# Optimization experiments

Measured on AMD Instinct MI355X. Metric: run time of the kernel, lower is better.

## Reference

```python
import jax, jax.numpy as jnp
import numpy as np

B, NA, NB = 2, 2048, 2048
DIM_A, DIM_B = 256, 256
HEADS, DH_A, DH_B = 8, 64, 64
INNER_A, INNER_B = DH_A * HEADS, DH_B * HEADS
EPS = 1e-5


def layer_norm(x, w, b):
    m = jnp.mean(x, axis=-1, keepdims=True)
    v = jnp.mean(jnp.square(x - m), axis=-1, keepdims=True)
    return (x - m) * jax.lax.rsqrt(v + EPS) * w + b


def setup_inputs() -> dict:
    key = jax.random.key(0)
    ks = jax.random.split(key, 16)
    s = 0.02
    return {
        "feat_a": jax.random.normal(ks[0], (B, NA, DIM_A), jnp.float32),
        "feat_b": jax.random.normal(ks[1], (B, NB, DIM_B), jnp.float32),
        "mask_a_b": jax.random.bernoulli(ks[2], 0.5, (B, NA, NB)),
        # linear weights stored (in, out)
        "Wq": jax.random.normal(ks[3], (DIM_A, INNER_B), jnp.float32) * s,
        "bq": jnp.zeros((INNER_B,), jnp.float32),
        "Wk": jax.random.normal(ks[4], (DIM_B, INNER_B), jnp.float32) * s,
        "bk": jnp.zeros((INNER_B,), jnp.float32),
        "Wv": jax.random.normal(ks[5], (DIM_B, INNER_A), jnp.float32) * s,
        "bv": jnp.zeros((INNER_A,), jnp.float32),
        "Wg": jax.random.normal(ks[6], (DIM_A, INNER_A), jnp.float32) * s,
        "bg": jnp.zeros((INNER_A,), jnp.float32),
        "Wo": jax.random.normal(ks[7], (INNER_A, DIM_A), jnp.float32) * s,
        "bo": jnp.zeros((DIM_A,), jnp.float32),
        "ln_a_w": jnp.ones((DIM_A,), jnp.float32),
        "ln_a_b": jnp.zeros((DIM_A,), jnp.float32),
        "ln_b_w": jnp.ones((DIM_B,), jnp.float32),
        "ln_b_b": jnp.zeros((DIM_B,), jnp.float32),
        "qln_w": jnp.ones((INNER_B,), jnp.float32),
        "qln_b": jnp.zeros((INNER_B,), jnp.float32),
        "kln_w": jnp.ones((INNER_B,), jnp.float32),
        "kln_b": jnp.zeros((INNER_B,), jnp.float32),
    }


def reference(feat_a, feat_b, mask_a_b, Wq, bq, Wk, bk, Wv, bv, Wg, bg, Wo, bo,
              ln_a_w, ln_a_b, ln_b_w, ln_b_b, qln_w, qln_b, kln_w, kln_b):
    scale = DH_B ** -0.5
    fa = layer_norm(feat_a, ln_a_w, ln_a_b)            # (b, na, dim_a)
    fb = layer_norm(feat_b, ln_b_w, ln_b_b)            # (b, nb, dim_b)
    q = layer_norm(fa @ Wq + bq, qln_w, qln_b)         # (b, na, inner_b)
    k = layer_norm(fb @ Wk + bk, kln_w, kln_b)         # (b, nb, inner_b)
    v = fb @ Wv + bv                                   # (b, nb, inner_a)
    g = fa @ Wg + bg                                   # (b, na, inner_a)
    q = q.reshape(B, NA, HEADS, DH_B)
    k = k.reshape(B, NB, HEADS, DH_B)
    v = v.reshape(B, NB, HEADS, DH_A)
    g = g.reshape(B, NA, HEADS, DH_A)
    sim = jnp.einsum('bihd,bjhd->bhij', q, k) * scale  # (b, h, na, nb)
    neg = jnp.finfo(sim.dtype).min
    sim = jnp.where(mask_a_b[:, None, :, :], sim, neg)
    attn = jax.nn.softmax(sim, axis=-1)
    out = jnp.einsum('bhij,bjhd->bihd', attn, v)       # (b, na, h, dh_a)
    out = jax.nn.sigmoid(g) * out
    out = out.reshape(B, NA, INNER_A)
    return out @ Wo + bo                               # (b, na, dim_a)
```

## Files before the change

### kernel.cpp

```cpp
#include <hip/hip_runtime.h>
#include <hip/hip_bf16.h>

using bf16 = __hip_bfloat16;
typedef short bf16x8 __attribute__((ext_vector_type(8)));
typedef float f32x4 __attribute__((ext_vector_type(4)));
typedef unsigned short ushort8_t __attribute__((ext_vector_type(8)));
typedef unsigned long long u64;

static constexpr int NA_ = 2048, NB_ = 2048;
static constexpr int H_ = 8, DH_ = 64, INNER_ = 512;
static constexpr int MROWS = 2 * NA_;

#define MFMA32(a, b, c) __builtin_amdgcn_mfma_f32_16x16x32_bf16(a, b, c, 0, 0, 0)

__device__ __forceinline__ unsigned short bfbits(float x) {
  bf16 h = __float2bfloat16(x);
  return __builtin_bit_cast(unsigned short, h);
}
__device__ __forceinline__ float b2f(unsigned short u) {
  unsigned v = ((unsigned)u) << 16;
  return __builtin_bit_cast(float, v);
}

__global__ __launch_bounds__(256) void prep_kernel(
    const float* __restrict__ fa_in, const float* __restrict__ fb_in,
    const float* __restrict__ law, const float* __restrict__ lab,
    const float* __restrict__ lbw, const float* __restrict__ lbb,
    bf16* __restrict__ fa, bf16* __restrict__ fb,
    const float* __restrict__ Wq, const float* __restrict__ Wk,
    const float* __restrict__ Wv, const float* __restrict__ Wg,
    const float* __restrict__ Wo,
    bf16* __restrict__ Wqt, bf16* __restrict__ Wkt,
    bf16* __restrict__ Wvt, bf16* __restrict__ Wgt,
    bf16* __restrict__ Woth, bf16* __restrict__ Wotl,
    const void* __restrict__ maskp, u64* __restrict__ mbits) {
  int blk = blockIdx.x;
  int t = threadIdx.x;
  if (blk < 2048) {
    int row = blk * 4 + (t >> 6);
    int lane = t & 63;
    const float *src, *w, *bb;
    bf16* dst;
    int r;
    if (row < MROWS) { src = fa_in; w = law; bb = lab; dst = fa; r = row; }
    else             { src = fb_in; w = lbw; bb = lbb; dst = fb; r = row - MROWS; }
    float4 x = *(const float4*)(src + (size_t)r * 256 + lane * 4);
    float s  = (x.x + x.y) + (x.z + x.w);
    float s2 = (x.x * x.x + x.y * x.y) + (x.z * x.z + x.w * x.w);
#pragma unroll
    for (int m = 32; m >= 1; m >>= 1) { s += __shfl_xor(s, m); s2 += __shfl_xor(s2, m); }
    float mean = s * (1.0f / 256.0f);
    float var  = s2 * (1.0f / 256.0f) - mean * mean;
    float rstd = rsqrtf(var + 1e-5f);
    float4 wv = *(const float4*)(w + lane * 4);
    float4 bv = *(const float4*)(bb + lane * 4);
    ushort4 o;
    o.x = bfbits((x.x - mean) * rstd * wv.x + bv.x);
    o.y = bfbits((x.y - mean) * rstd * wv.y + bv.y);
    o.z = bfbits((x.z - mean) * rstd * wv.z + bv.z);
    o.w = bfbits((x.w - mean) * rstd * wv.w + bv.w);
    *(ushort4*)(dst + (size_t)r * 256 + lane * 4) = o;
  } else if (blk < 4608) {
    int z = (blk - 2048) >> 9;
    int idx = ((blk - 2048) & 511) * 256 + t;
    if (z < 4) {
      const float* W = (z == 0) ? Wq : (z == 1) ? Wk : (z == 2) ? Wv : Wg;
      bf16* Wt = (z == 0) ? Wqt : (z == 1) ? Wkt : (z == 2) ? Wvt : Wgt;
      int kk = idx >> 9, n = idx & 511;
      Wt[n * 256 + kk] = __float2bfloat16(W[idx]);
    } else {
      int kk = idx >> 8, n = idx & 255;
      float w = Wo[idx];
      bf16 hi = __float2bfloat16(w);
      Woth[n * 512 + kk] = hi;
      Wotl[n * 512 + kk] = __float2bfloat16(w - __bfloat162float(hi));
    }
  } else {
    __shared__ unsigned shf[4];
    const unsigned char* mu = (const unsigned char*)maskp;
    bool nz = ((t & 3) != 0) && (mu[t] != 0);
    u64 bal = __ballot(nz);
    if ((t & 63) == 0) shf[t >> 6] = (bal != 0ull) ? 1u : 0u;
    __syncthreads();
    bool m8 = (shf[0] | shf[1] | shf[2] | shf[3]) != 0;
    int lane = t & 63, wid = t >> 6;
    int lb = blk - 4608;
    for (size_t word = (size_t)lb * 4 + wid; word < 131072; word += 8192) {
      size_t e = word * 64 + lane;
      int v = m8 ? (int)mu[e] : ((const int*)maskp)[e];
      u64 b2 = __ballot(v != 0);
      if (lane == 0) mbits[word] = b2;
    }
  }
}

__global__ __launch_bounds__(256) void gemm4_kernel(
    const bf16* __restrict__ fa, const bf16* __restrict__ fb,
    const bf16* __restrict__ Wqt, const bf16* __restrict__ Wkt,
    const bf16* __restrict__ Wgt, const bf16* __restrict__ Wvt,
    const float* __restrict__ bq, const float* __restrict__ bk,
    const float* __restrict__ bg, const float* __restrict__ bv,
    const float* __restrict__ qlw, const float* __restrict__ qlb,
    const float* __restrict__ klw, const float* __restrict__ klb,
    bf16* __restrict__ qo, bf16* __restrict__ ko,
    bf16* __restrict__ gout, bf16* __restrict__ vout) {
  __shared__ __align__(16) char sm[27648];
  int z = blockIdx.z;
  int t = threadIdx.x, wave = t >> 6, lane = t & 63;
  int lm = lane & 15, quad = lane >> 4, q8 = quad * 8;

  if (z < 2) {
    bf16* As = (bf16*)sm;
    float* Pred = (float*)(sm + 16896);
    float* MV   = (float*)(sm + 17408);
    const bf16* A    = z ? fb : fa;
    const bf16* Wt   = z ? Wkt : Wqt;
    const float* bias = z ? bk : bq;
    const float* lw  = z ? klw : qlw;
    const float* lb  = z ? klb : qlb;
    bf16* out        = z ? ko : qo;
    int m0 = blockIdx.x * 16;
#pragma unroll
    for (int i = 0; i < 2; i++) {
      int id = t + 256 * i, r = id >> 5, cg = id & 31;
      *(ushort8_t*)(&As[r * 264 + cg * 8]) =
          *(const ushort8_t*)(A + (size_t)(m0 + r) * 256 + cg * 8);
    }
    __syncthreads();
    int n0w = wave * 128;
    f32x4 acc[8] = {};
    const bf16* wrow[8];
#pragma unroll
    for (int ni = 0; ni < 8; ni++) wrow[ni] = Wt + (size_t)(n0w + ni * 16 + lm) * 256;
#pragma unroll
    for (int ks = 0; ks < 8; ks++) {
      int k0 = ks * 32;
      bf16x8 af = *(const bf16x8*)(&As[lm * 264 + k0 + q8]);
#pragma unroll
      for (int ni = 0; ni < 8; ni++) {
        bf16x8 bf_ = *(const bf16x8*)(wrow[ni] + k0 + q8);
        acc[ni] = MFMA32(af, bf_, acc[ni]);
      }
    }
    float bvv[8];
#pragma unroll
    for (int ni = 0; ni < 8; ni++) bvv[ni] = bias[n0w + ni * 16 + lm];
#pragma unroll
    for (int ni = 0; ni < 8; ni++)
#pragma unroll
      for (int r = 0; r < 4; r++) acc[ni][r] += bvv[ni];
#pragma unroll
    for (int r = 0; r < 4; r++) {
      float s = 0.f, s2 = 0.f;
#pragma unroll
      for (int ni = 0; ni < 8; ni++) { s += acc[ni][r]; s2 += acc[ni][r] * acc[ni][r]; }
#pragma unroll
      for (int m = 1; m <= 8; m <<= 1) { s += __shfl_xor(s, m); s2 += __shfl_xor(s2, m); }
      if (lm == 0) {
        int row = quad * 4 + r;
        Pred[row * 8 + wave * 2]     = s;
        Pred[row * 8 + wave * 2 + 1] = s2;
      }
    }
    __syncthreads();
    if (t < 16) {
      float s = 0.f, s2 = 0.f;
#pragma unroll
      for (int w = 0; w < 4; w++) { s += Pred[t * 8 + w * 2]; s2 += Pred[t * 8 + w * 2 + 1]; }
      float mean = s * (1.0f / 512.0f);
      float var  = s2 * (1.0f / 512.0f) - mean * mean;
      MV[t * 2]     = mean;
      MV[t * 2 + 1] = rsqrtf(var + 1e-5f);
    }
    __syncthreads();
    float lww[8], lbb_[8];
#pragma unroll
    for (int ni = 0; ni < 8; ni++) {
      lww[ni]  = lw[n0w + ni * 16 + lm];
      lbb_[ni] = lb[n0w + ni * 16 + lm];
    }
#pragma unroll
    for (int r = 0; r < 4; r++) {
      int row = quad * 4 + r;
      float mean = MV[row * 2], rstd = MV[row * 2 + 1];
      size_t obase = (size_t)(m0 + row) * 512 + n0w;
#pragma unroll
      for (int ni = 0; ni < 8; ni++)
        out[obase + ni * 16 + lm] =
            __float2bfloat16((acc[ni][r] - mean) * rstd * lww[ni] + lbb_[ni]);
    }
  } else {
    bf16* As = (bf16*)sm;
    bf16* Bs = (bf16*)(sm + 18432);
    const bf16* A    = (z == 3) ? fb : fa;
    const bf16* Wt   = (z == 3) ? Wvt : Wgt;
    const float* bias = (z == 3) ? bv : bg;
    int x = blockIdx.x;
    int m0 = (x >> 3) * 128, n0 = (x & 7) * 64;
    int wm = wave * 32;
    f32x4 acc[2][4] = {};
    for (int k0 = 0; k0 < 256; k0 += 64) {
      __syncthreads();
#pragma unroll
      for (int i = 0; i < 4; i++) {
        int id = t + 256 * i, r = id >> 3, cg = id & 7;
        *(ushort8_t*)(&As[r * 72 + cg * 8]) =
            *(const ushort8_t*)(A + (size_t)(m0 + r) * 256 + k0 + cg * 8);
      }
#pragma unroll
      for (int i = 0; i < 2; i++) {
        int id = t + 256 * i, r = id >> 3, cg = id & 7;
        *(ushort8_t*)(&Bs[r * 72 + cg * 8]) =
            *(const ushort8_t*)(Wt + (size_t)(n0 + r) * 256 + k0 + cg * 8);
      }
      __syncthreads();
#pragma unroll
      for (int kk = 0; kk < 64; kk += 32) {
        bf16x8 af[2], bf_[4];
#pragma unroll
        for (int mi = 0; mi < 2; mi++)
          af[mi] = *(const bf16x8*)(&As[(wm + mi * 16 + lm) * 72 + kk + q8]);
#pragma unroll
        for (int ni = 0; ni < 4; ni++)
          bf_[ni] = *(const bf16x8*)(&Bs[(ni * 16 + lm) * 72 + kk + q8]);
#pragma unroll
        for (int mi = 0; mi < 2; mi++)
#pragma unroll
          for (int ni = 0; ni < 4; ni++)
            acc[mi][ni] = MFMA32(af[mi], bf_[ni], acc[mi][ni]);
      }
    }
    if (z == 2) {
#pragma unroll
      for (int mi = 0; mi < 2; mi++)
#pragma unroll
        for (int ni = 0; ni < 4; ni++) {
          int nn = n0 + ni * 16 + lm;
          float bvv = bias[nn];
          int mb = m0 + wm + mi * 16 + quad * 4;
#pragma unroll
          for (int r = 0; r < 4; r++)
            gout[(size_t)(mb + r) * 512 + nn] = __float2bfloat16(acc[mi][ni][r] + bvv);
        }
    } else {
      __syncthreads();
      bf16* buf = (bf16*)sm;
#pragma unroll
      for (int mi = 0; mi < 2; mi++)
#pragma unroll
        for (int ni = 0; ni < 4; ni++) {
          int d_local = ni * 16 + lm;
          float bvv = bias[n0 + d_local];
          int j_local = wm + mi * 16 + quad * 4;
#pragma unroll
          for (int r = 0; r < 4; r++)
            buf[d_local * 136 + j_local + r] = __float2bfloat16(acc[mi][ni][r] + bvv);
        }
      __syncthreads();
      int bidx2 = m0 >> 11, j0g = m0 & 2047, hh = n0 >> 6;
      int dl = t >> 2, jseg = (t & 3) * 32;
      bf16* dstrow = vout + (size_t)((bidx2 * 8 + hh) * 64 + dl) * 2048 + j0g + jseg;
#pragma unroll
      for (int c = 0; c < 4; c++)
        *(ushort8_t*)(dstrow + c * 8) = *(const ushort8_t*)(&buf[dl * 136 + jseg + c * 8]);
    }
  }
}

__global__ __launch_bounds__(512) void attn_kernel(
    const bf16* __restrict__ q, const bf16* __restrict__ k,
    const bf16* __restrict__ vt, const bf16* __restrict__ g,
    const u64* __restrict__ mbits,
    bf16* __restrict__ gh, bf16* __restrict__ gl) {
  __shared__ __align__(16) char smem[65024];
  bf16* Qs = (bf16*)smem;
  bf16* KsB = (bf16*)(smem + 9216);
  bf16* VsB = (bf16*)(smem + 27648);
  bf16* PsB = (bf16*)(smem + 46080);
  float* Om = (float*)(smem + 9216);
  float* Lbuf = (float*)(smem + 64512);

  int qt = blockIdx.x, bh = blockIdx.y;
  int bidx = bh >> 3, h = bh & 7;
  int i0 = qt * 64;
  int t = threadIdx.x, wave = t >> 6, lane = t & 63;
  int jhalf = wave >> 2, w4 = wave & 3;
  int lm = lane & 15, quad = lane >> 4, q8 = quad * 8;
  int lt = t & 255;

  {
    int r = t >> 3, cg = t & 7;
    *(ushort8_t*)(&Qs[r * 72 + cg * 8]) =
        *(const ushort8_t*)(q + (size_t)(bidx * NA_ + i0 + r) * INNER_ + h * DH_ + cg * 8);
  }
  __syncthreads();
  bf16x8 bq0 = *(const bf16x8*)(&Qs[(w4 * 16 + lm) * 72 + q8]);
  bf16x8 bq1 = *(const bf16x8*)(&Qs[(w4 * 16 + lm) * 72 + 32 + q8]);

  f32x4 oacc[4] = {};
  float psum = 0.f;
  const float scale2 = 0.125f * 1.44269504088896f;

  const bf16* kb = k + (size_t)(bidx * NB_) * INNER_ + h * DH_;
  const bf16* vb = vt + (size_t)(bh * DH_) * NB_;
  bf16* Pw = PsB + wave * (16 * 72);
  bf16* Ks = KsB + jhalf * (64 * 72);
  bf16* Vs = VsB + jhalf * (64 * 72);
  const u64* mrp = mbits + ((size_t)(bidx * NA_ + i0 + w4 * 16 + lm)) * (NB_ / 64) + jhalf * 16;

  for (int it = 0; it < 16; it++) {
    int j0 = jhalf * 1024 + it * 64;
    __syncthreads();
#pragma unroll
    for (int i = 0; i < 2; i++) {
      int id = lt + 256 * i, r = id >> 3, cg = id & 7;
      *(ushort8_t*)(&Ks[r * 72 + cg * 8]) =
          *(const ushort8_t*)(kb + (size_t)(j0 + r) * INNER_ + cg * 8);
      *(ushort8_t*)(&Vs[r * 72 + cg * 8]) =
          *(const ushort8_t*)(vb + (size_t)r * NB_ + j0 + cg * 8);
    }
    u64 sm = mrp[it] >> (quad * 4);
    __syncthreads();

    f32x4 st[4];
#pragma unroll
    for (int nt = 0; nt < 4; nt++) {
      bf16x8 a0 = *(const bf16x8*)(&Ks[(nt * 16 + lm) * 72 + q8]);
      bf16x8 a1 = *(const bf16x8*)(&Ks[(nt * 16 + lm) * 72 + 32 + q8]);
      f32x4 a = {0.f, 0.f, 0.f, 0.f};
      a = MFMA32(a0, bq0, a);
      a = MFMA32(a1, bq1, a);
      st[nt] = a;
    }

    float pr[4][4];
#pragma unroll
    for (int nt = 0; nt < 4; nt++)
#pragma unroll
      for (int r = 0; r < 4; r++) {
        float p = exp2f(st[nt][r] * scale2 - 16.0f);
        unsigned live = (unsigned)(sm >> (nt * 16 + r)) & 1u;
        pr[nt][r] = live ? p : 0.0f;
      }

    float s0 = (pr[0][0] + pr[0][1]) + (pr[0][2] + pr[0][3]);
    float s1 = (pr[1][0] + pr[1][1]) + (pr[1][2] + pr[1][3]);
    float s2 = (pr[2][0] + pr[2][1]) + (pr[2][2] + pr[2][3]);
    float s3 = (pr[3][0] + pr[3][1]) + (pr[3][2] + pr[3][3]);
    psum += (s0 + s1) + (s2 + s3);

#pragma unroll
    for (int nt = 0; nt < 4; nt++) {
      ushort4 pk;
      pk.x = bfbits(pr[nt][0]);
      pk.y = bfbits(pr[nt][1]);
      pk.z = bfbits(pr[nt][2]);
      pk.w = bfbits(pr[nt][3]);
      *(ushort4*)(Pw + lm * 72 + nt * 16 + quad * 4) = pk;
    }

    bf16x8 ap0 = *(const bf16x8*)(&Pw[lm * 72 + q8]);
    bf16x8 ap1 = *(const bf16x8*)(&Pw[lm * 72 + 32 + q8]);
#pragma unroll
    for (int c = 0; c < 4; c++) {
      bf16x8 v0 = *(const bf16x8*)(&Vs[(c * 16 + lm) * 72 + q8]);
      bf16x8 v1 = *(const bf16x8*)(&Vs[(c * 16 + lm) * 72 + 32 + q8]);
      oacc[c] = MFMA32(ap0, v0, oacc[c]);
      oacc[c] = MFMA32(ap1, v1, oacc[c]);
    }
  }

  psum += __shfl_xor(psum, 16);
  psum += __shfl_xor(psum, 32);

  __syncthreads();
  if (quad == 0) Lbuf[jhalf * 64 + w4 * 16 + lm] = psum;
  if (jhalf == 1) {
#pragma unroll
    for (int c = 0; c < 4; c++)
#pragma unroll
      for (int r = 0; r < 4; r++)
        Om[w4 * (16 * 66) + (quad * 4 + r) * 66 + c * 16 + lm] = oacc[c][r];
  }
  __syncthreads();
  if (jhalf == 0) {
    int mrow = i0 + w4 * 16 + quad * 4;
    float inv[4];
#pragma unroll
    for (int r = 0; r < 4; r++) {
      float l = Lbuf[w4 * 16 + quad * 4 + r] + Lbuf[64 + w4 * 16 + quad * 4 + r];
      inv[r] = 1.0f / l;
    }
#pragma unroll
    for (int c = 0; c < 4; c++) {
      int col = h * DH_ + c * 16 + lm;
#pragma unroll
      for (int r = 0; r < 4; r++) {
        float o = oacc[c][r] + Om[w4 * (16 * 66) + (quad * 4 + r) * 66 + c * 16 + lm];
        size_t idx = (size_t)(bidx * NA_ + mrow + r) * INNER_ + col;
        float gv = b2f(__builtin_bit_cast(unsigned short, g[idx]));
        float sig = 1.0f / (1.0f + __expf(-gv));
        float val = o * inv[r] * sig;
        unsigned short hb = bfbits(val);
        gh[idx] = __builtin_bit_cast(bf16, hb);
        gl[idx] = __float2bfloat16(val - b2f(hb));
      }
    }
  }
}

__global__ __launch_bounds__(256) void gemm_split_kernel(
    const bf16* __restrict__ Ah, const bf16* __restrict__ Al,
    const bf16* __restrict__ Bh, const bf16* __restrict__ Bl,
    const float* __restrict__ bias, float* __restrict__ C) {
  constexpr int K = 512, N = 256;
  __shared__ __align__(16) bf16 Ash[32 * 72];
  __shared__ __align__(16) bf16 Asl[32 * 72];
  __shared__ __align__(16) bf16 Bsh[64 * 72];
  __shared__ __align__(16) bf16 Bsl[64 * 72];
  int n0 = blockIdx.x * 64, m0 = blockIdx.y * 32;
  int t = threadIdx.x, wave = t >> 6, lane = t & 63;
  int lm = lane & 15, quad = lane >> 4, q8 = quad * 8;
  int wm = (wave & 1) * 16, wn = (wave >> 1) * 32;
  f32x4 acc[2] = {};
  for (int k0 = 0; k0 < K; k0 += 64) {
    __syncthreads();
    {
      int r = t >> 3, cg = t & 7;
      size_t ga = (size_t)(m0 + r) * K + k0 + cg * 8;
      *(ushort8_t*)(&Ash[r * 72 + cg * 8]) = *(const ushort8_t*)(Ah + ga);
      *(ushort8_t*)(&Asl[r * 72 + cg * 8]) = *(const ushort8_t*)(Al + ga);
    }
#pragma unroll
    for (int i = 0; i < 2; i++) {
      int id = t + 256 * i, r = id >> 3, cg = id & 7;
      size_t gb = (size_t)(n0 + r) * K + k0 + cg * 8;
      *(ushort8_t*)(&Bsh[r * 72 + cg * 8]) = *(const ushort8_t*)(Bh + gb);
      *(ushort8_t*)(&Bsl[r * 72 + cg * 8]) = *(const ushort8_t*)(Bl + gb);
    }
    __syncthreads();
#pragma unroll
    for (int kk = 0; kk < 64; kk += 32) {
      bf16x8 ah = *(const bf16x8*)(&Ash[(wm + lm) * 72 + kk + q8]);
      bf16x8 al = *(const bf16x8*)(&Asl[(wm + lm) * 72 + kk + q8]);
#pragma unroll
      for (int ni = 0; ni < 2; ni++) {
        bf16x8 bh_ = *(const bf16x8*)(&Bsh[(wn + ni * 16 + lm) * 72 + kk + q8]);
        bf16x8 bl_ = *(const bf16x8*)(&Bsl[(wn + ni * 16 + lm) * 72 + kk + q8]);
        acc[ni] = MFMA32(ah, bh_, acc[ni]);
        acc[ni] = MFMA32(ah, bl_, acc[ni]);
        acc[ni] = MFMA32(al, bh_, acc[ni]);
      }
    }
  }
#pragma unroll
  for (int ni = 0; ni < 2; ni++) {
    int n = n0 + wn + ni * 16 + lm;
    float bvv = bias[n];
    int mb = m0 + wm + quad * 4;
#pragma unroll
    for (int r = 0; r < 4; r++) C[(size_t)(mb + r) * N + n] = acc[ni][r] + bvv;
  }
}

extern "C" void kernel_launch(void* const* d_in, const int* in_sizes, int n_in,
                              void* d_out, int out_size, void* d_ws, size_t ws_size,
                              hipStream_t stream) {
  const float* feat_a = (const float*)d_in[0];
  const float* feat_b = (const float*)d_in[1];
  const void*  mask   = d_in[2];
  const float* Wq = (const float*)d_in[3];
  const float* bq = (const float*)d_in[4];
  const float* Wk = (const float*)d_in[5];
  const float* bk = (const float*)d_in[6];
  const float* Wv = (const float*)d_in[7];
  const float* bv = (const float*)d_in[8];
  const float* Wg = (const float*)d_in[9];
  const float* bg = (const float*)d_in[10];
  const float* Wo = (const float*)d_in[11];
  const float* bo = (const float*)d_in[12];
  const float* law = (const float*)d_in[13];
  const float* lab = (const float*)d_in[14];
  const float* lbw = (const float*)d_in[15];
  const float* lbb = (const float*)d_in[16];
  const float* qlw = (const float*)d_in[17];
  const float* qlb = (const float*)d_in[18];
  const float* klw = (const float*)d_in[19];
  const float* klb = (const float*)d_in[20];

  char* ws = (char*)d_ws;
  size_t off = 0;
  auto alloc = [&](size_t bytes) -> void* {
    void* p = ws + off;
    off += (bytes + 255) & ~(size_t)255;
    return p;
  };
  bf16* fa    = (bf16*)alloc((size_t)MROWS * 256 * 2);
  bf16* fb    = (bf16*)alloc((size_t)MROWS * 256 * 2);
  bf16* Wqt   = (bf16*)alloc((size_t)131072 * 2);
  bf16* Wkt   = (bf16*)alloc((size_t)131072 * 2);
  bf16* Wvt   = (bf16*)alloc((size_t)131072 * 2);
  bf16* Wgt   = (bf16*)alloc((size_t)131072 * 2);
  bf16* Woth  = (bf16*)alloc((size_t)131072 * 2);
  bf16* Wotl  = (bf16*)alloc((size_t)131072 * 2);
  bf16* qb_   = (bf16*)alloc((size_t)MROWS * 512 * 2);
  bf16* kb_   = (bf16*)alloc((size_t)MROWS * 512 * 2);
  bf16* vtb   = (bf16*)alloc((size_t)1024 * 2048 * 2);
  bf16* gbuf  = (bf16*)alloc((size_t)MROWS * 512 * 2);
  bf16* gh    = (bf16*)alloc((size_t)MROWS * 512 * 2);
  bf16* gl    = (bf16*)alloc((size_t)MROWS * 512 * 2);
  u64*  mbits = (u64*)alloc((size_t)131072 * 8);

  prep_kernel<<<6656, 256, 0, stream>>>(
      feat_a, feat_b, law, lab, lbw, lbb, fa, fb,
      Wq, Wk, Wv, Wg, Wo, Wqt, Wkt, Wvt, Wgt, Woth, Wotl, mask, mbits);
  gemm4_kernel<<<dim3(256, 1, 4), 256, 0, stream>>>(
      fa, fb, Wqt, Wkt, Wgt, Wvt, bq, bk, bg, bv,
      qlw, qlb, klw, klb, qb_, kb_, gbuf, vtb);
  attn_kernel<<<dim3(32, 16), 512, 0, stream>>>(qb_, kb_, vtb, gbuf, mbits, gh, gl);
  gemm_split_kernel<<<dim3(4, 128), 256, 0, stream>>>(gh, gl, Woth, Wotl, bo, (float*)d_out);
}
```

Baseline: 204.0 us.

## Rewrite attention kernel with 32x32x16 MFMA, register-shuffled P, and four-way key split

Restructures the attention kernel so each wave computes a 32x32 score tile with the 32x32x16 bf16 MFMA. Probabilities are passed to the PV product through cross-lane shuffles instead of a shared-memory round trip. Keys are split four ways across waves, with 128-key tiles, a transposed V layout, and a two-level shared-memory reduction of partial outputs. The gated hi/lo outputs are now staged through LDS for coalesced 16-byte stores, and an occupancy hint is added. The exp2 bias offset is dropped, which could risk overflow for large unnormalized scores.

```diff
diff --git a/kernel.cpp b/kernel.cpp
--- a/kernel.cpp
+++ b/kernel.cpp
@@ -4,6 +4,7 @@
 using bf16 = __hip_bfloat16;
 typedef short bf16x8 __attribute__((ext_vector_type(8)));
 typedef float f32x4 __attribute__((ext_vector_type(4)));
+typedef float f32x16 __attribute__((ext_vector_type(16)));
 typedef unsigned short ushort8_t __attribute__((ext_vector_type(8)));
 typedef unsigned long long u64;
 
@@ -12,6 +13,7 @@
 static constexpr int MROWS = 2 * NA_;
 
 #define MFMA32(a, b, c) __builtin_amdgcn_mfma_f32_16x16x32_bf16(a, b, c, 0, 0, 0)
+#define MFMA3216(a, b, c) __builtin_amdgcn_mfma_f32_32x32x16_bf16(a, b, c, 0, 0, 0)
 
 __device__ __forceinline__ unsigned short bfbits(float x) {
   bf16 h = __float2bfloat16(x);
@@ -267,145 +269,227 @@
   }
 }
 
-__global__ __launch_bounds__(512) void attn_kernel(
+__global__ __launch_bounds__(512, 4) void attn_kernel(
     const bf16* __restrict__ q, const bf16* __restrict__ k,
     const bf16* __restrict__ vt, const bf16* __restrict__ g,
     const u64* __restrict__ mbits,
     bf16* __restrict__ gh, bf16* __restrict__ gl) {
-  __shared__ __align__(16) char smem[65024];
-  bf16* Qs = (bf16*)smem;
-  bf16* KsB = (bf16*)(smem + 9216);
-  bf16* VsB = (bf16*)(smem + 27648);
-  bf16* PsB = (bf16*)(smem + 46080);
-  float* Om = (float*)(smem + 9216);
-  float* Lbuf = (float*)(smem + 64512);
+  __shared__ __align__(16) char smem[46080];
+  bf16* Ks = (bf16*)smem;
+  bf16* Vs = (bf16*)(smem + 18432);
+  bf16* Qs = (bf16*)(smem + 35840);
+  float* Lbuf = (float*)(smem + 45056);
+  float* OmA = (float*)smem;
+  bf16* Tbuf = (bf16*)(smem + 35840);
 
   int qt = blockIdx.x, bh = blockIdx.y;
-  int bidx = bh >> 3, h = bh & 7;
+  int bidx = bh >> 3, hh = bh & 7;
   int i0 = qt * 64;
-  int t = threadIdx.x, wave = t >> 6, lane = t & 63;
-  int jhalf = wave >> 2, w4 = wave & 3;
-  int lm = lane & 15, quad = lane >> 4, q8 = quad * 8;
-  int lt = t & 255;
+  int t = threadIdx.x, w = t >> 6, lane = t & 63;
+  int ig = w & 1, js = w >> 1;
+  int l31 = lane & 31, hf = lane >> 5;
 
   {
     int r = t >> 3, cg = t & 7;
     *(ushort8_t*)(&Qs[r * 72 + cg * 8]) =
-        *(const ushort8_t*)(q + (size_t)(bidx * NA_ + i0 + r) * INNER_ + h * DH_ + cg * 8);
-  }
-  __syncthreads();
-  bf16x8 bq0 = *(const bf16x8*)(&Qs[(w4 * 16 + lm) * 72 + q8]);
-  bf16x8 bq1 = *(const bf16x8*)(&Qs[(w4 * 16 + lm) * 72 + 32 + q8]);
-
-  f32x4 oacc[4] = {};
+        *(const ushort8_t*)(q + (size_t)(bidx * NA_ + i0 + r) * INNER_ + hh * DH_ + cg * 8);
+  }
+  __syncthreads();
+  bf16x8 bq[4];
+#pragma unroll
+  for (int kt = 0; kt < 4; kt++)
+    bq[kt] = *(const bf16x8*)(&Qs[(ig * 32 + l31) * 72 + kt * 16 + hf * 8]);
+
+  f32x16 oT[2];
+#pragma unroll
+  for (int i = 0; i < 16; i++) { oT[0][i] = 0.f; oT[1][i] = 0.f; }
   float psum = 0.f;
   const float scale2 = 0.125f * 1.44269504088896f;
 
-  const bf16* kb = k + (size_t)(bidx * NB_) * INNER_ + h * DH_;
+  const bf16* kb = k + (size_t)(bidx * NB_) * INNER_ + hh * DH_;
   const bf16* vb = vt + (size_t)(bh * DH_) * NB_;
-  bf16* Pw = PsB + wave * (16 * 72);
-  bf16* Ks = KsB + jhalf * (64 * 72);
-  bf16* Vs = VsB + jhalf * (64 * 72);
-  const u64* mrp = mbits + ((size_t)(bidx * NA_ + i0 + w4 * 16 + lm)) * (NB_ / 64) + jhalf * 16;
+  const u64* mrp = mbits + (size_t)(bidx * NA_ + i0 + ig * 32 + l31) * (NB_ / 64);
+  int msh = (js & 1) * 32 + hf * 4;
 
   for (int it = 0; it < 16; it++) {
-    int j0 = jhalf * 1024 + it * 64;
+    int j0 = it * 128;
     __syncthreads();
 #pragma unroll
     for (int i = 0; i < 2; i++) {
-      int id = lt + 256 * i, r = id >> 3, cg = id & 7;
-      *(ushort8_t*)(&Ks[r * 72 + cg * 8]) =
-          *(const ushort8_t*)(kb + (size_t)(j0 + r) * INNER_ + cg * 8);
-      *(ushort8_t*)(&Vs[r * 72 + cg * 8]) =
-          *(const ushort8_t*)(vb + (size_t)r * NB_ + j0 + cg * 8);
-    }
-    u64 sm = mrp[it] >> (quad * 4);
-    __syncthreads();
-
-    f32x4 st[4];
-#pragma unroll
-    for (int nt = 0; nt < 4; nt++) {
-      bf16x8 a0 = *(const bf16x8*)(&Ks[(nt * 16 + lm) * 72 + q8]);
-      bf16x8 a1 = *(const bf16x8*)(&Ks[(nt * 16 + lm) * 72 + 32 + q8]);
-      f32x4 a = {0.f, 0.f, 0.f, 0.f};
-      a = MFMA32(a0, bq0, a);
-      a = MFMA32(a1, bq1, a);
-      st[nt] = a;
-    }
-
-    float pr[4][4];
-#pragma unroll
-    for (int nt = 0; nt < 4; nt++)
-#pragma unroll
-      for (int r = 0; r < 4; r++) {
-        float p = exp2f(st[nt][r] * scale2 - 16.0f);
-        unsigned live = (unsigned)(sm >> (nt * 16 + r)) & 1u;
-        pr[nt][r] = live ? p : 0.0f;
-      }
-
-    float s0 = (pr[0][0] + pr[0][1]) + (pr[0][2] + pr[0][3]);
-    float s1 = (pr[1][0] + pr[1][1]) + (pr[1][2] + pr[1][3]);
-    float s2 = (pr[2][0] + pr[2][1]) + (pr[2][2] + pr[2][3]);
-    float s3 = (pr[3][0] + pr[3][1]) + (pr[3][2] + pr[3][3]);
-    psum += (s0 + s1) + (s2 + s3);
-
-#pragma unroll
-    for (int nt = 0; nt < 4; nt++) {
-      ushort4 pk;
-      pk.x = bfbits(pr[nt][0]);
-      pk.y = bfbits(pr[nt][1]);
-      pk.z = bfbits(pr[nt][2]);
-      pk.w = bfbits(pr[nt][3]);
-      *(ushort4*)(Pw + lm * 72 + nt * 16 + quad * 4) = pk;
-    }
-
-    bf16x8 ap0 = *(const bf16x8*)(&Pw[lm * 72 + q8]);
-    bf16x8 ap1 = *(const bf16x8*)(&Pw[lm * 72 + 32 + q8]);
-#pragma unroll
-    for (int c = 0; c < 4; c++) {
-      bf16x8 v0 = *(const bf16x8*)(&Vs[(c * 16 + lm) * 72 + q8]);
-      bf16x8 v1 = *(const bf16x8*)(&Vs[(c * 16 + lm) * 72 + 32 + q8]);
-      oacc[c] = MFMA32(ap0, v0, oacc[c]);
-      oacc[c] = MFMA32(ap1, v1, oacc[c]);
-    }
-  }
-
-  psum += __shfl_xor(psum, 16);
+      int id = t + 512 * i;
+      {
+        int r = id >> 3, cg = id & 7;
+        *(ushort8_t*)(&Ks[r * 72 + cg * 8]) =
+            *(const ushort8_t*)(kb + (size_t)(j0 + r) * INNER_ + cg * 8);
+      }
+      {
+        int d = id >> 4, jg = id & 15;
+        *(ushort8_t*)(&Vs[d * 136 + jg * 8]) =
+            *(const ushort8_t*)(vb + (size_t)d * NB_ + j0 + jg * 8);
+      }
+    }
+    u64 wm_ = mrp[it * 2 + (js >> 1)];
+    __syncthreads();
+
+    f32x16 st;
+#pragma unroll
+    for (int i = 0; i < 16; i++) st[i] = 0.f;
+#pragma unroll
+    for (int kt = 0; kt < 4; kt++) {
+      bf16x8 ka = *(const bf16x8*)(&Ks[(js * 32 + l31) * 72 + kt * 16 + hf * 8]);
+      st = MFMA3216(ka, bq[kt], st);
+    }
+
+    unsigned mlo = (unsigned)(wm_ >> msh);
+    float pr[16];
+#pragma unroll
+    for (int reg = 0; reg < 16; reg++) {
+      float p = exp2f(st[reg] * scale2);
+      unsigned bitpos = (unsigned)((reg & 3) + 8 * (reg >> 2));
+      pr[reg] = ((mlo >> bitpos) & 1u) ? p : 0.f;
+    }
+#pragma unroll
+    for (int i = 0; i < 16; i += 4)
+      psum += ((pr[i] + pr[i + 1]) + (pr[i + 2] + pr[i + 3]));
+    unsigned dw[8];
+#pragma unroll
+    for (int p = 0; p < 8; p++)
+      dw[p] = (unsigned)bfbits(pr[2 * p]) | ((unsigned)bfbits(pr[2 * p + 1]) << 16);
+
+    unsigned rx[8];
+#pragma unroll
+    for (int p = 0; p < 8; p++) rx[p] = (unsigned)__shfl_xor((int)dw[p], 32);
+    unsigned f0[4], f1[4];
+    if (hf == 0) {
+      f0[0] = dw[0]; f0[1] = dw[1]; f0[2] = rx[0]; f0[3] = rx[1];
+      f1[0] = dw[4]; f1[1] = dw[5]; f1[2] = rx[4]; f1[3] = rx[5];
+    } else {
+      f0[0] = rx[2]; f0[1] = rx[3]; f0[2] = dw[2]; f0[3] = dw[3];
+      f1[0] = rx[6]; f1[1] = rx[7]; f1[2] = dw[6]; f1[3] = dw[7];
+    }
+    bf16x8 pf0 = __builtin_bit_cast(bf16x8, *(uint4*)f0);
+    bf16x8 pf1 = __builtin_bit_cast(bf16x8, *(uint4*)f1);
+
+#pragma unroll
+    for (int dt = 0; dt < 2; dt++) {
+      bf16x8 va0 = *(const bf16x8*)(&Vs[(dt * 32 + l31) * 136 + js * 32 + hf * 8]);
+      bf16x8 va1 = *(const bf16x8*)(&Vs[(dt * 32 + l31) * 136 + js * 32 + 16 + hf * 8]);
+      oT[dt] = MFMA3216(va0, pf0, oT[dt]);
+      oT[dt] = MFMA3216(va1, pf1, oT[dt]);
+    }
+  }
+
   psum += __shfl_xor(psum, 32);
 
   __syncthreads();
-  if (quad == 0) Lbuf[jhalf * 64 + w4 * 16 + lm] = psum;
-  if (jhalf == 1) {
-#pragma unroll
-    for (int c = 0; c < 4; c++)
-#pragma unroll
-      for (int r = 0; r < 4; r++)
-        Om[w4 * (16 * 66) + (quad * 4 + r) * 66 + c * 16 + lm] = oacc[c][r];
-  }
-  __syncthreads();
-  if (jhalf == 0) {
-    int mrow = i0 + w4 * 16 + quad * 4;
-    float inv[4];
-#pragma unroll
-    for (int r = 0; r < 4; r++) {
-      float l = Lbuf[w4 * 16 + quad * 4 + r] + Lbuf[64 + w4 * 16 + quad * 4 + r];
-      inv[r] = 1.0f / l;
-    }
-#pragma unroll
-    for (int c = 0; c < 4; c++) {
-      int col = h * DH_ + c * 16 + lm;
-#pragma unroll
-      for (int r = 0; r < 4; r++) {
-        float o = oacc[c][r] + Om[w4 * (16 * 66) + (quad * 4 + r) * 66 + c * 16 + lm];
-        size_t idx = (size_t)(bidx * NA_ + mrow + r) * INNER_ + col;
-        float gv = b2f(__builtin_bit_cast(unsigned short, g[idx]));
-        float sig = 1.0f / (1.0f + __expf(-gv));
-        float val = o * inv[r] * sig;
-        unsigned short hb = bfbits(val);
-        gh[idx] = __builtin_bit_cast(bf16, hb);
-        gl[idx] = __float2bfloat16(val - b2f(hb));
-      }
-    }
+  if (lane < 32) Lbuf[js * 64 + ig * 32 + l31] = psum;
+  if (js & 1) {
+    float* B = OmA + (size_t)(ig * 2 + (js >> 1)) * 2112;
+#pragma unroll
+    for (int dt = 0; dt < 2; dt++)
+#pragma unroll
+      for (int reg = 0; reg < 16; reg++) {
+        int d = dt * 32 + (reg & 3) + 8 * (reg >> 2) + 4 * hf;
+        B[d * 33 + l31] = oT[dt][reg];
+      }
+  }
+  __syncthreads();
+  if (!(js & 1)) {
+    float* B = OmA + (size_t)(ig * 2 + (js >> 1)) * 2112;
+#pragma unroll
+    for (int dt = 0; dt < 2; dt++)
+#pragma unroll
+      for (int reg = 0; reg < 16; reg++) {
+        int d = dt * 32 + (reg & 3) + 8 * (reg >> 2) + 4 * hf;
+        oT[dt][reg] += B[d * 33 + l31];
+      }
+  }
+  __syncthreads();
+  if (js == 2) {
+    float* B = OmA + (size_t)(ig * 2 + 1) * 2112;
+#pragma unroll
+    for (int dt = 0; dt < 2; dt++)
+#pragma unroll
+      for (int reg = 0; reg < 16; reg++) {
+        int d = dt * 32 + (reg & 3) + 8 * (reg >> 2) + 4 * hf;
+        B[d * 33 + l31] = oT[dt][reg];
+      }
+  }
+  __syncthreads();
+  if (js == 0) {
+    float* B = OmA + (size_t)(ig * 2 + 1) * 2112;
+#pragma unroll
+    for (int dt = 0; dt < 2; dt++)
+#pragma unroll
+      for (int reg = 0; reg < 16; reg++) {
+        int d = dt * 32 + (reg & 3) + 8 * (reg >> 2) + 4 * hf;
+        oT[dt][reg] += B[d * 33 + l31];
+      }
+    int il = ig * 32 + l31;
+    float l = ((Lbuf[il] + Lbuf[64 + il]) + (Lbuf[128 + il] + Lbuf[192 + il]));
+    float inv = 1.0f / l;
+    size_t gpb = (size_t)(bidx * NA_ + i0 + il) * INNER_ + hh * DH_;
+#pragma unroll
+    for (int dt = 0; dt < 2; dt++)
+#pragma unroll
+      for (int rg = 0; rg < 4; rg++) {
+        int dbase = dt * 32 + rg * 8 + hf * 4;
+        short4 g4 = *(const short4*)(g + gpb + dbase);
+        unsigned short gu[4] = {(unsigned short)g4.x, (unsigned short)g4.y,
+                                (unsigned short)g4.z, (unsigned short)g4.w};
+#pragma unroll
+        for (int rr = 0; rr < 4; rr++) {
+          float gvf = b2f(gu[rr]);
+          float sig = 1.0f / (1.0f + __expf(-gvf));
+          oT[dt][rg * 4 + rr] = oT[dt][rg * 4 + rr] * inv * sig;
+        }
+      }
+  }
+  __syncthreads();
+  if (js == 0) {
+    int il = ig * 32 + l31;
+#pragma unroll
+    for (int dt = 0; dt < 2; dt++)
+#pragma unroll
+      for (int rg = 0; rg < 4; rg++) {
+        int dbase = dt * 32 + rg * 8 + hf * 4;
+        unsigned w0 = (unsigned)bfbits(oT[dt][rg * 4 + 0]) |
+                      ((unsigned)bfbits(oT[dt][rg * 4 + 1]) << 16);
+        unsigned w1 = (unsigned)bfbits(oT[dt][rg * 4 + 2]) |
+                      ((unsigned)bfbits(oT[dt][rg * 4 + 3]) << 16);
+        *(unsigned*)(&Tbuf[il * 72 + dbase])     = w0;
+        *(unsigned*)(&Tbuf[il * 72 + dbase + 2]) = w1;
+      }
+  }
+  __syncthreads();
+  {
+    int ri = t >> 3, seg = t & 7;
+    ushort8_t v = *(const ushort8_t*)(&Tbuf[ri * 72 + seg * 8]);
+    *(ushort8_t*)(gh + (size_t)(bidx * NA_ + i0 + ri) * INNER_ + hh * DH_ + seg * 8) = v;
+  }
+  __syncthreads();
+  if (js == 0) {
+    int il = ig * 32 + l31;
+#pragma unroll
+    for (int dt = 0; dt < 2; dt++)
+#pragma unroll
+      for (int rg = 0; rg < 4; rg++) {
+        int dbase = dt * 32 + rg * 8 + hf * 4;
+        unsigned short lo[4];
+#pragma unroll
+        for (int rr = 0; rr < 4; rr++) {
+          float v = oT[dt][rg * 4 + rr];
+          lo[rr] = bfbits(v - b2f(bfbits(v)));
+        }
+        *(unsigned*)(&Tbuf[il * 72 + dbase])     = (unsigned)lo[0] | ((unsigned)lo[1] << 16);
+        *(unsigned*)(&Tbuf[il * 72 + dbase + 2]) = (unsigned)lo[2] | ((unsigned)lo[3] << 16);
+      }
+  }
+  __syncthreads();
+  {
+    int ri = t >> 3, seg = t & 7;
+    ushort8_t v = *(const ushort8_t*)(&Tbuf[ri * 72 + seg * 8]);
+    *(ushort8_t*)(gl + (size_t)(bidx * NA_ + i0 + ri) * INNER_ + hh * DH_ + seg * 8) = v;
   }
 }
 
```

Measured after the change: 205.5 us. No clear change (+0.8%).
